# Performance work log

Hardware: AMD Instinct MI355X
Metric: run time of the kernel (lower is better)

## Reference

```python
import jax, jax.numpy as jnp
import numpy as np

N, E, F_IN, H, G, C = 50000, 600000, 128, 128, 500, 10


def _lin(k, fi, fo):
    # Glorot-ish scaled init for a [fi, fo] weight
    return (jax.random.normal(k, (fi, fo), jnp.float32) / np.float32(np.sqrt(fi)))


def setup_inputs() -> dict:
    key = jax.random.key(0)
    ks = jax.random.split(key, 16)
    x = jax.random.normal(ks[0], (N, F_IN), jnp.float32)
    edge_index = jax.random.randint(ks[1], (2, E), 0, N, dtype=jnp.int32)
    batch = jnp.sort(jax.random.randint(ks[2], (N,), 0, G, dtype=jnp.int32))
    return {
        "x": x, "edge_index": edge_index, "batch": batch,
        # SAGEConv i: out = mean_aggr @ Wl + bl + x @ Wr  (PyG default: mean aggr, root weight, bias on lin_l)
        "Wl1": _lin(ks[3], F_IN, H), "bl1": jnp.zeros((H,), jnp.float32), "Wr1": _lin(ks[4], F_IN, H),
        "Wl2": _lin(ks[5], H, H),    "bl2": jnp.zeros((H,), jnp.float32), "Wr2": _lin(ks[6], H, H),
        "Wl3": _lin(ks[7], H, H),    "bl3": jnp.zeros((H,), jnp.float32), "Wr3": _lin(ks[8], H, H),
        "W4": _lin(ks[9], H, 64), "b4": jnp.zeros((64,), jnp.float32),
        "W5": _lin(ks[10], 64, C), "b5": jnp.zeros((C,), jnp.float32),
    }


def _segment_mean(vals, ids, num_segments):
    s = jax.ops.segment_sum(vals, ids, num_segments=num_segments)
    cnt = jax.ops.segment_sum(jnp.ones((vals.shape[0], 1), vals.dtype), ids, num_segments=num_segments)
    return s / jnp.maximum(cnt, 1.0)


def _sage_conv(x, src, dst, Wl, bl, Wr):
    # gather source features along edges, mean-aggregate at destinations
    aggr = _segment_mean(x[src], dst, N)  # [N, F]
    return aggr @ Wl + bl + x @ Wr


def reference(x, edge_index, batch, Wl1, bl1, Wr1, Wl2, bl2, Wr2, Wl3, bl3, Wr3, W4, b4, W5, b5):
    src, dst = edge_index[0], edge_index[1]
    h = jax.nn.relu(_sage_conv(x, src, dst, Wl1, bl1, Wr1))
    h = jax.nn.relu(_sage_conv(h, src, dst, Wl2, bl2, Wr2))
    h = jax.nn.relu(_sage_conv(h, src, dst, Wl3, bl3, Wr3))
    g = _segment_mean(h, batch, G)          # global mean pool -> [G, H]
    g = jax.nn.relu(g @ W4 + b4)
    return jax.nn.log_softmax(g @ W5 + b5, axis=-1)
```

## Files before the change

kernel.cpp:

```cpp
#include <hip/hip_runtime.h>
#include <hip/hip_bf16.h>
#include <math.h>

#define FH 128

typedef __attribute__((ext_vector_type(8))) short short8v;
typedef __attribute__((ext_vector_type(4))) float float4v;
typedef unsigned short ushort_t;
typedef unsigned int   uint32;

__device__ __forceinline__ ushort_t f2bf(float f) {
    uint32 u = __builtin_bit_cast(uint32, f);
    u += 0x7fffu + ((u >> 16) & 1u);
    return (ushort_t)(u >> 16);
}
__device__ __forceinline__ float bf_lo(uint32 w) { return __builtin_bit_cast(float, w << 16); }
__device__ __forceinline__ float bf_hi(uint32 w) { return __builtin_bit_cast(float, w & 0xffff0000u); }
__device__ __forceinline__ uint32 pack2(float lo, float hi) {
    return (uint32)f2bf(lo) | ((uint32)f2bf(hi) << 16);
}

__device__ __forceinline__ void pack_one(const float* __restrict__ Wl,
                                         const float* __restrict__ Wr,
                                         ushort_t* __restrict__ Bp, int t) {
    int k = t >> 7, n = t & 127;
    float v = (k < FH) ? Wl[k * FH + n] : Wr[(k - FH) * FH + n];
    int nt = n >> 4, kt = k >> 5;
    int lane = (n & 15) + (((k >> 3) & 3) << 4);
    int j = k & 7;
    Bp[(((nt * 8 + kt) * 64) + lane) * 8 + j] = f2bf(v);
}

__global__ __launch_bounds__(256) void prep_kernel(const float* __restrict__ x,
                                                   ushort_t* __restrict__ xb, size_t n,
                                                   int cvtBlocks,
                                                   const float* __restrict__ Wl1, const float* __restrict__ Wr1, ushort_t* __restrict__ Bp1,
                                                   const float* __restrict__ Wl2, const float* __restrict__ Wr2, ushort_t* __restrict__ Bp2,
                                                   const float* __restrict__ Wl3, const float* __restrict__ Wr3, ushort_t* __restrict__ Bp3) {
    int b = blockIdx.x;
    if (b < cvtBlocks) {
        size_t base = ((size_t)b * 256 + threadIdx.x) * 8;
        if (base >= n) return;
        const float4 a = *(const float4*)(x + base);
        const float4 c = *(const float4*)(x + base + 4);
        ushort_t o[8] = {f2bf(a.x), f2bf(a.y), f2bf(a.z), f2bf(a.w),
                         f2bf(c.x), f2bf(c.y), f2bf(c.z), f2bf(c.w)};
        *(uint4*)(xb + base) = *(const uint4*)o;
    } else {
        int pb = b - cvtBlocks;
        int which = pb >> 7;
        int t = (pb & 127) * 256 + threadIdx.x;
        if (which == 0)      pack_one(Wl1, Wr1, Bp1, t);
        else if (which == 1) pack_one(Wl2, Wr2, Bp2, t);
        else                 pack_one(Wl3, Wr3, Bp3, t);
    }
}

__global__ __launch_bounds__(256) void deg_kernel(const int* __restrict__ dst,
                                                  int* __restrict__ deg, int E) {
    int e = blockIdx.x * 256 + threadIdx.x;
    if (e < E) atomicAdd(&deg[dst[e]], 1);
}

__global__ __launch_bounds__(256) void scan1_kernel(const int* __restrict__ deg,
                                                    int* __restrict__ rowptr,
                                                    int* __restrict__ blockSums, int N) {
    __shared__ int lds[256];
    const int base = blockIdx.x * 1024;
    const int t = threadIdx.x;
    int v[4]; int sum = 0;
    #pragma unroll
    for (int j = 0; j < 4; ++j) {
        int idx = base + t * 4 + j;
        v[j] = (idx < N) ? deg[idx] : 0;
        sum += v[j];
    }
    lds[t] = sum; __syncthreads();
    for (int off = 1; off < 256; off <<= 1) {
        int val = lds[t];
        int add = (t >= off) ? lds[t - off] : 0;
        __syncthreads();
        lds[t] = val + add;
        __syncthreads();
    }
    int run = (t > 0) ? lds[t - 1] : 0;
    #pragma unroll
    for (int j = 0; j < 4; ++j) {
        int idx = base + t * 4 + j;
        if (idx < N) rowptr[idx] = run;
        run += v[j];
    }
    if (t == 255) blockSums[blockIdx.x] = lds[255];
}

__global__ void scan2_kernel(int* __restrict__ blockSums, int* __restrict__ rowptr,
                             int nb, int N) {
    if (threadIdx.x == 0 && blockIdx.x == 0) {
        int carry = 0;
        for (int i = 0; i < nb; ++i) {
            int s = blockSums[i];
            blockSums[i] = carry;
            carry += s;
        }
        rowptr[N] = carry;
    }
}

__global__ __launch_bounds__(256) void scan3_kernel(int* __restrict__ rowptr,
                                                    int* __restrict__ pos,
                                                    const int* __restrict__ blockSums, int N) {
    const int base = blockIdx.x * 1024;
    const int add = blockSums[blockIdx.x];
    #pragma unroll
    for (int j = 0; j < 4; ++j) {
        int idx = base + threadIdx.x * 4 + j;
        if (idx < N) {
            int v = rowptr[idx] + add;
            rowptr[idx] = v;
            pos[idx] = v;
        }
    }
}

__global__ __launch_bounds__(256) void fill_csr_kernel(const int* __restrict__ src,
                                                       const int* __restrict__ dst,
                                                       int* __restrict__ pos,
                                                       int* __restrict__ csr, int E) {
    int e = blockIdx.x * 256 + threadIdx.x;
    if (e >= E) return;
    int idx = atomicAdd(&pos[dst[e]], 1);
    csr[idx] = src[e];
}

__global__ __launch_bounds__(256) void group_bounds_kernel(const int* __restrict__ batch,
                                                           int* __restrict__ gstart,
                                                           int N, int G) {
    int g = blockIdx.x * 256 + threadIdx.x;
    if (g > G) return;
    int lo = 0, hi = N;
    while (lo < hi) {
        int mid = (lo + hi) >> 1;
        if (batch[mid] < g) lo = mid + 1; else hi = mid;
    }
    gstart[g] = lo;
}

__global__ __launch_bounds__(256) void pull_mean_kernel(const ushort_t* __restrict__ x,
                                                        const int* __restrict__ rowptr,
                                                        const int* __restrict__ csr,
                                                        ushort_t* __restrict__ aggr, int N) {
    const int v = (blockIdx.x * 256 + threadIdx.x) >> 6;
    if (v >= N) return;
    const int lane = threadIdx.x & 63;
    const int grp  = lane >> 4;
    const int li   = lane & 15;
    const int beg = rowptr[v], end = rowptr[v + 1];
    const uint4* xp = (const uint4*)x + li;

    float a0 = 0.f, a1 = 0.f, a2 = 0.f, a3 = 0.f;
    float a4 = 0.f, a5 = 0.f, a6 = 0.f, a7 = 0.f;

    int i = beg + grp;
    for (; i + 4 < end; i += 8) {
        const int s0 = csr[i];
        const int s1 = csr[i + 4];
        const uint4 w0 = xp[(size_t)s0 * 16];
        const uint4 w1 = xp[(size_t)s1 * 16];
        a0 += bf_lo(w0.x); a1 += bf_hi(w0.x); a2 += bf_lo(w0.y); a3 += bf_hi(w0.y);
        a4 += bf_lo(w0.z); a5 += bf_hi(w0.z); a6 += bf_lo(w0.w); a7 += bf_hi(w0.w);
        a0 += bf_lo(w1.x); a1 += bf_hi(w1.x); a2 += bf_lo(w1.y); a3 += bf_hi(w1.y);
        a4 += bf_lo(w1.z); a5 += bf_hi(w1.z); a6 += bf_lo(w1.w); a7 += bf_hi(w1.w);
    }
    if (i < end) {
        const int s0 = csr[i];
        const uint4 w0 = xp[(size_t)s0 * 16];
        a0 += bf_lo(w0.x); a1 += bf_hi(w0.x); a2 += bf_lo(w0.y); a3 += bf_hi(w0.y);
        a4 += bf_lo(w0.z); a5 += bf_hi(w0.z); a6 += bf_lo(w0.w); a7 += bf_hi(w0.w);
    }

    a0 += __shfl_xor(a0, 16); a1 += __shfl_xor(a1, 16);
    a2 += __shfl_xor(a2, 16); a3 += __shfl_xor(a3, 16);
    a4 += __shfl_xor(a4, 16); a5 += __shfl_xor(a5, 16);
    a6 += __shfl_xor(a6, 16); a7 += __shfl_xor(a7, 16);
    a0 += __shfl_xor(a0, 32); a1 += __shfl_xor(a1, 32);
    a2 += __shfl_xor(a2, 32); a3 += __shfl_xor(a3, 32);
    a4 += __shfl_xor(a4, 32); a5 += __shfl_xor(a5, 32);
    a6 += __shfl_xor(a6, 32); a7 += __shfl_xor(a7, 32);

    if (grp == 0) {
        const float inv = 1.0f / (float)max(end - beg, 1);
        uint4 o;
        o.x = pack2(a0 * inv, a1 * inv);
        o.y = pack2(a2 * inv, a3 * inv);
        o.z = pack2(a4 * inv, a5 * inv);
        o.w = pack2(a6 * inv, a7 * inv);
        ((uint4*)aggr)[(size_t)v * 16 + li] = o;
    }
}

__global__ __launch_bounds__(256) void sage_mfma_kernel(const ushort_t* __restrict__ xin,
                                                        const ushort_t* __restrict__ aggr,
                                                        const ushort_t* __restrict__ Bp,
                                                        const float* __restrict__ bl,
                                                        ushort_t* __restrict__ out, int M) {
    __shared__ ushort_t sB[8 * 8 * 64 * 8];
    const int tid = threadIdx.x;
    {
        const uint4* s = (const uint4*)Bp;
        uint4* d = (uint4*)sB;
        #pragma unroll
        for (int i = 0; i < 16; ++i)
            d[tid + 256 * i] = s[tid + 256 * i];
    }
    __syncthreads();

    const int wave = tid >> 6;
    const int lane = tid & 63;
    const int grp  = lane >> 4;
    const int rowBase = (blockIdx.x * 4 + wave) * 16;
    if (rowBase >= M) return;
    const int arow = min(rowBase + (lane & 15), M - 1);

    short8v afrag[8];
    #pragma unroll
    for (int kt = 0; kt < 4; ++kt)
        afrag[kt] = *(const short8v*)(aggr + (size_t)arow * FH + kt * 32 + grp * 8);
    #pragma unroll
    for (int kt = 0; kt < 4; ++kt)
        afrag[4 + kt] = *(const short8v*)(xin + (size_t)arow * FH + kt * 32 + grp * 8);

    #pragma unroll
    for (int nt = 0; nt < 8; ++nt) {
        float4v acc = {0.f, 0.f, 0.f, 0.f};
        #pragma unroll
        for (int kt = 0; kt < 8; ++kt) {
            const short8v b = *(const short8v*)(sB + (((nt * 8 + kt) * 64) + lane) * 8);
            acc = __builtin_amdgcn_mfma_f32_16x16x32_bf16(afrag[kt], b, acc, 0, 0, 0);
        }
        const int col = nt * 16 + (lane & 15);
        const float bias = bl[col];
        #pragma unroll
        for (int r = 0; r < 4; ++r) {
            const int row = rowBase + grp * 4 + r;
            if (row < M)
                out[(size_t)row * FH + col] = f2bf(fmaxf(acc[r] + bias, 0.f));
        }
    }
}

__global__ __launch_bounds__(256) void head_kernel(const ushort_t* __restrict__ h,
                                                   const int* __restrict__ gstart,
                                                   const float* __restrict__ W4,
                                                   const float* __restrict__ b4,
                                                   const float* __restrict__ W5,
                                                   const float* __restrict__ b5,
                                                   float* __restrict__ out, int G) {
    __shared__ float sred[4][FH];
    __shared__ float sg2[64];
    __shared__ float sl[10];
    __shared__ float slse;
    const int g = blockIdx.x;
    const int t = threadIdx.x;
    const int wave = t >> 6, lane = t & 63;
    const int beg = gstart[g], end = gstart[g + 1];

    const uint32* hp = (const uint32*)h + lane;
    float a0 = 0.f, a1 = 0.f;
    for (int i = beg + wave; i < end; i += 4) {
        const uint32 w = hp[(size_t)i * 64];
        a0 += bf_lo(w); a1 += bf_hi(w);
    }
    sred[wave][lane * 2]     = a0;
    sred[wave][lane * 2 + 1] = a1;
    __syncthreads();
    if (t < FH) {
        const float s = sred[0][t] + sred[1][t] + sred[2][t] + sred[3][t];
        sred[0][t] = s / (float)max(end - beg, 1);
    }
    __syncthreads();
    if (t < 64) {
        float acc = b4[t];
        #pragma unroll 4
        for (int k = 0; k < FH; ++k)
            acc += sred[0][k] * W4[k * 64 + t];
        sg2[t] = fmaxf(acc, 0.f);
    }
    __syncthreads();
    if (t < 10) {
        float acc = b5[t];
        #pragma unroll 4
        for (int k = 0; k < 64; ++k)
            acc += sg2[k] * W5[k * 10 + t];
        sl[t] = acc;
    }
    __syncthreads();
    if (t == 0) {
        float m = sl[0];
        #pragma unroll
        for (int j = 1; j < 10; ++j) m = fmaxf(m, sl[j]);
        float s = 0.f;
        #pragma unroll
        for (int j = 0; j < 10; ++j) s += expf(sl[j] - m);
        slse = m + logf(s);
    }
    __syncthreads();
    if (t < 10) out[g * 10 + t] = sl[t] - slse;
}

extern "C" void kernel_launch(void* const* d_in, const int* in_sizes, int n_in,
                              void* d_out, int out_size, void* d_ws, size_t ws_size,
                              hipStream_t stream) {
    const float* x     = (const float*)d_in[0];
    const int*   ei    = (const int*)d_in[1];
    const int*   batch = (const int*)d_in[2];
    const float* Wl1 = (const float*)d_in[3];
    const float* bl1 = (const float*)d_in[4];
    const float* Wr1 = (const float*)d_in[5];
    const float* Wl2 = (const float*)d_in[6];
    const float* bl2 = (const float*)d_in[7];
    const float* Wr2 = (const float*)d_in[8];
    const float* Wl3 = (const float*)d_in[9];
    const float* bl3 = (const float*)d_in[10];
    const float* Wr3 = (const float*)d_in[11];
    const float* W4  = (const float*)d_in[12];
    const float* b4  = (const float*)d_in[13];
    const float* W5  = (const float*)d_in[14];
    const float* b5  = (const float*)d_in[15];
    float* out = (float*)d_out;

    const int N = in_sizes[0] / FH;
    const int E = in_sizes[1] / 2;
    const int G = out_size / 10;
    const int* src = ei;
    const int* dst = ei + E;

    char* p = (char*)d_ws;
    auto take = [&](size_t bytes) { char* q = p; p += (bytes + 255) & ~(size_t)255; return q; };
    ushort_t* xb    = (ushort_t*)take((size_t)N * FH * 2);
    ushort_t* h     = (ushort_t*)take((size_t)N * FH * 2);
    ushort_t* aggrb = (ushort_t*)take((size_t)N * FH * 2);
    int* deg        = (int*)take((size_t)N * 4);
    int* rowptr     = (int*)take((size_t)(N + 1) * 4);
    int* pos        = (int*)take((size_t)N * 4);
    int* csr        = (int*)take((size_t)E * 4);
    int* blockSums  = (int*)take(256 * 4);
    ushort_t* Bp1   = (ushort_t*)take(256 * FH * 2);
    ushort_t* Bp2   = (ushort_t*)take(256 * FH * 2);
    ushort_t* Bp3   = (ushort_t*)take(256 * FH * 2);
    int* gstart     = (int*)take((size_t)(G + 1) * 4);

    const int nb = (N + 1023) / 1024;

    hipMemsetAsync(deg, 0, (size_t)N * 4, stream);

    const int cvtBlocks = (int)(((size_t)N * FH / 8 + 255) / 256);
    prep_kernel<<<cvtBlocks + 384, 256, 0, stream>>>(x, xb, (size_t)N * FH, cvtBlocks,
                                                     Wl1, Wr1, Bp1, Wl2, Wr2, Bp2, Wl3, Wr3, Bp3);

    deg_kernel<<<(E + 255) / 256, 256, 0, stream>>>(dst, deg, E);
    scan1_kernel<<<nb, 256, 0, stream>>>(deg, rowptr, blockSums, N);
    scan2_kernel<<<1, 64, 0, stream>>>(blockSums, rowptr, nb, N);
    scan3_kernel<<<nb, 256, 0, stream>>>(rowptr, pos, blockSums, N);
    fill_csr_kernel<<<(E + 255) / 256, 256, 0, stream>>>(src, dst, pos, csr, E);

    group_bounds_kernel<<<(G + 256) / 256, 256, 0, stream>>>(batch, gstart, N, G);

    const int pullGrid = (N * 64 + 255) / 256;
    const int gemmGrid = (N + 63) / 64;

    pull_mean_kernel<<<pullGrid, 256, 0, stream>>>(xb, rowptr, csr, aggrb, N);
    sage_mfma_kernel<<<gemmGrid, 256, 0, stream>>>(xb, aggrb, Bp1, bl1, h, N);

    pull_mean_kernel<<<pullGrid, 256, 0, stream>>>(h, rowptr, csr, aggrb, N);
    sage_mfma_kernel<<<gemmGrid, 256, 0, stream>>>(h, aggrb, Bp2, bl2, h, N);

    pull_mean_kernel<<<pullGrid, 256, 0, stream>>>(h, rowptr, csr, aggrb, N);
    sage_mfma_kernel<<<gemmGrid, 256, 0, stream>>>(h, aggrb, Bp3, bl3, h, N);

    head_kernel<<<G, 256, 0, stream>>>(h, gstart, W4, b4, W5, b5, out, G);
}
```

Before: 242.9 us.

## Fuse setup kernels, prefetch gathers in pull-mean, stage GEMM output through LDS

Folds the degree-count and group-bounds kernels into the prep kernel to cut launches. The pull-mean aggregation now issues up to four independent neighbour gathers per lane group before accumulating, to raise memory-level parallelism for typical degrees. The MFMA kernel keeps all output tiles in registers, then writes bias+ReLU results into LDS and stores full 16-byte rows for coalesced global writes. This costs a block barrier and more accumulator registers.

New measurement: 219.6 us. 9.6% less time.

```diff
diff --git a/kernel.cpp b/kernel.cpp
--- a/kernel.cpp
+++ b/kernel.cpp
@@ -31,12 +31,13 @@
     Bp[(((nt * 8 + kt) * 64) + lane) * 8 + j] = f2bf(v);
 }
 
-__global__ __launch_bounds__(256) void prep_kernel(const float* __restrict__ x,
-                                                   ushort_t* __restrict__ xb, size_t n,
-                                                   int cvtBlocks,
-                                                   const float* __restrict__ Wl1, const float* __restrict__ Wr1, ushort_t* __restrict__ Bp1,
-                                                   const float* __restrict__ Wl2, const float* __restrict__ Wr2, ushort_t* __restrict__ Bp2,
-                                                   const float* __restrict__ Wl3, const float* __restrict__ Wr3, ushort_t* __restrict__ Bp3) {
+__global__ __launch_bounds__(256) void fused_prep_kernel(
+        const float* __restrict__ x, ushort_t* __restrict__ xb, size_t n, int cvtBlocks,
+        const float* __restrict__ Wl1, const float* __restrict__ Wr1, ushort_t* __restrict__ Bp1,
+        const float* __restrict__ Wl2, const float* __restrict__ Wr2, ushort_t* __restrict__ Bp2,
+        const float* __restrict__ Wl3, const float* __restrict__ Wr3, ushort_t* __restrict__ Bp3,
+        const int* __restrict__ dst, int* __restrict__ deg, int E, int degBlocks,
+        const int* __restrict__ batch, int* __restrict__ gstart, int N, int G) {
     int b = blockIdx.x;
     if (b < cvtBlocks) {
         size_t base = ((size_t)b * 256 + threadIdx.x) * 8;
@@ -46,20 +47,34 @@
         ushort_t o[8] = {f2bf(a.x), f2bf(a.y), f2bf(a.z), f2bf(a.w),
                          f2bf(c.x), f2bf(c.y), f2bf(c.z), f2bf(c.w)};
         *(uint4*)(xb + base) = *(const uint4*)o;
-    } else {
-        int pb = b - cvtBlocks;
-        int which = pb >> 7;
-        int t = (pb & 127) * 256 + threadIdx.x;
+        return;
+    }
+    b -= cvtBlocks;
+    if (b < 384) {
+        int which = b >> 7;
+        int t = (b & 127) * 256 + threadIdx.x;
         if (which == 0)      pack_one(Wl1, Wr1, Bp1, t);
         else if (which == 1) pack_one(Wl2, Wr2, Bp2, t);
         else                 pack_one(Wl3, Wr3, Bp3, t);
-    }
-}
-
-__global__ __launch_bounds__(256) void deg_kernel(const int* __restrict__ dst,
-                                                  int* __restrict__ deg, int E) {
-    int e = blockIdx.x * 256 + threadIdx.x;
-    if (e < E) atomicAdd(&deg[dst[e]], 1);
+        return;
+    }
+    b -= 384;
+    if (b < degBlocks) {
+        int e = b * 256 + threadIdx.x;
+        if (e < E) atomicAdd(&deg[dst[e]], 1);
+        return;
+    }
+    b -= degBlocks;
+    {
+        int g = b * 256 + threadIdx.x;
+        if (g > G) return;
+        int lo = 0, hi = N;
+        while (lo < hi) {
+            int mid = (lo + hi) >> 1;
+            if (batch[mid] < g) lo = mid + 1; else hi = mid;
+        }
+        gstart[g] = lo;
+    }
 }
 
 __global__ __launch_bounds__(256) void scan1_kernel(const int* __restrict__ deg,
@@ -130,19 +145,6 @@
     if (e >= E) return;
     int idx = atomicAdd(&pos[dst[e]], 1);
     csr[idx] = src[e];
-}
-
-__global__ __launch_bounds__(256) void group_bounds_kernel(const int* __restrict__ batch,
-                                                           int* __restrict__ gstart,
-                                                           int N, int G) {
-    int g = blockIdx.x * 256 + threadIdx.x;
-    if (g > G) return;
-    int lo = 0, hi = N;
-    while (lo < hi) {
-        int mid = (lo + hi) >> 1;
-        if (batch[mid] < g) lo = mid + 1; else hi = mid;
-    }
-    gstart[g] = lo;
 }
 
 __global__ __launch_bounds__(256) void pull_mean_kernel(const ushort_t* __restrict__ x,
@@ -157,25 +159,27 @@
     const int beg = rowptr[v], end = rowptr[v + 1];
     const uint4* xp = (const uint4*)x + li;
 
-    float a0 = 0.f, a1 = 0.f, a2 = 0.f, a3 = 0.f;
-    float a4 = 0.f, a5 = 0.f, a6 = 0.f, a7 = 0.f;
-
-    int i = beg + grp;
-    for (; i + 4 < end; i += 8) {
-        const int s0 = csr[i];
-        const int s1 = csr[i + 4];
-        const uint4 w0 = xp[(size_t)s0 * 16];
-        const uint4 w1 = xp[(size_t)s1 * 16];
-        a0 += bf_lo(w0.x); a1 += bf_hi(w0.x); a2 += bf_lo(w0.y); a3 += bf_hi(w0.y);
-        a4 += bf_lo(w0.z); a5 += bf_hi(w0.z); a6 += bf_lo(w0.w); a7 += bf_hi(w0.w);
-        a0 += bf_lo(w1.x); a1 += bf_hi(w1.x); a2 += bf_lo(w1.y); a3 += bf_hi(w1.y);
-        a4 += bf_lo(w1.z); a5 += bf_hi(w1.z); a6 += bf_lo(w1.w); a7 += bf_hi(w1.w);
-    }
-    if (i < end) {
-        const int s0 = csr[i];
-        const uint4 w0 = xp[(size_t)s0 * 16];
-        a0 += bf_lo(w0.x); a1 += bf_hi(w0.x); a2 += bf_lo(w0.y); a3 += bf_hi(w0.y);
-        a4 += bf_lo(w0.z); a5 += bf_hi(w0.z); a6 += bf_lo(w0.w); a7 += bf_hi(w0.w);
+    const uint4 z = {0u, 0u, 0u, 0u};
+    uint4 w0 = z, w1 = z, w2 = z, w3 = z;
+    const int i0 = beg + grp;
+    if (i0 < end)      w0 = xp[(size_t)csr[i0] * 16];
+    if (i0 + 4 < end)  w1 = xp[(size_t)csr[i0 + 4] * 16];
+    if (i0 + 8 < end)  w2 = xp[(size_t)csr[i0 + 8] * 16];
+    if (i0 + 12 < end) w3 = xp[(size_t)csr[i0 + 12] * 16];
+
+    float a0 = (bf_lo(w0.x) + bf_lo(w1.x)) + (bf_lo(w2.x) + bf_lo(w3.x));
+    float a1 = (bf_hi(w0.x) + bf_hi(w1.x)) + (bf_hi(w2.x) + bf_hi(w3.x));
+    float a2 = (bf_lo(w0.y) + bf_lo(w1.y)) + (bf_lo(w2.y) + bf_lo(w3.y));
+    float a3 = (bf_hi(w0.y) + bf_hi(w1.y)) + (bf_hi(w2.y) + bf_hi(w3.y));
+    float a4 = (bf_lo(w0.z) + bf_lo(w1.z)) + (bf_lo(w2.z) + bf_lo(w3.z));
+    float a5 = (bf_hi(w0.z) + bf_hi(w1.z)) + (bf_hi(w2.z) + bf_hi(w3.z));
+    float a6 = (bf_lo(w0.w) + bf_lo(w1.w)) + (bf_lo(w2.w) + bf_lo(w3.w));
+    float a7 = (bf_hi(w0.w) + bf_hi(w1.w)) + (bf_hi(w2.w) + bf_hi(w3.w));
+
+    for (int i = beg + 16 + grp; i < end; i += 4) {
+        const uint4 w = xp[(size_t)csr[i] * 16];
+        a0 += bf_lo(w.x); a1 += bf_hi(w.x); a2 += bf_lo(w.y); a3 += bf_hi(w.y);
+        a4 += bf_lo(w.z); a5 += bf_hi(w.z); a6 += bf_lo(w.w); a7 += bf_hi(w.w);
     }
 
     a0 += __shfl_xor(a0, 16); a1 += __shfl_xor(a1, 16);
@@ -198,12 +202,13 @@
     }
 }
 
+#define SO_STRIDE 136
 __global__ __launch_bounds__(256) void sage_mfma_kernel(const ushort_t* __restrict__ xin,
                                                         const ushort_t* __restrict__ aggr,
                                                         const ushort_t* __restrict__ Bp,
                                                         const float* __restrict__ bl,
                                                         ushort_t* __restrict__ out, int M) {
-    __shared__ ushort_t sB[8 * 8 * 64 * 8];
+    __shared__ ushort_t sB[32768];
     const int tid = threadIdx.x;
     {
         const uint4* s = (const uint4*)Bp;
@@ -217,9 +222,9 @@
     const int wave = tid >> 6;
     const int lane = tid & 63;
     const int grp  = lane >> 4;
+    const int li   = lane & 15;
     const int rowBase = (blockIdx.x * 4 + wave) * 16;
-    if (rowBase >= M) return;
-    const int arow = min(rowBase + (lane & 15), M - 1);
+    const int arow = min(rowBase + li, M - 1);
 
     short8v afrag[8];
     #pragma unroll
@@ -229,21 +234,36 @@
     for (int kt = 0; kt < 4; ++kt)
         afrag[4 + kt] = *(const short8v*)(xin + (size_t)arow * FH + kt * 32 + grp * 8);
 
+    float4v acc[8];
     #pragma unroll
     for (int nt = 0; nt < 8; ++nt) {
-        float4v acc = {0.f, 0.f, 0.f, 0.f};
+        acc[nt] = (float4v){0.f, 0.f, 0.f, 0.f};
         #pragma unroll
         for (int kt = 0; kt < 8; ++kt) {
             const short8v b = *(const short8v*)(sB + (((nt * 8 + kt) * 64) + lane) * 8);
-            acc = __builtin_amdgcn_mfma_f32_16x16x32_bf16(afrag[kt], b, acc, 0, 0, 0);
+            acc[nt] = __builtin_amdgcn_mfma_f32_16x16x32_bf16(afrag[kt], b, acc[nt], 0, 0, 0);
         }
-        const int col = nt * 16 + (lane & 15);
-        const float bias = bl[col];
+    }
+
+    __syncthreads();
+
+    ushort_t* so = sB + wave * (16 * SO_STRIDE);
+    #pragma unroll
+    for (int nt = 0; nt < 8; ++nt) {
+        const float bias = bl[nt * 16 + li];
         #pragma unroll
-        for (int r = 0; r < 4; ++r) {
-            const int row = rowBase + grp * 4 + r;
-            if (row < M)
-                out[(size_t)row * FH + col] = f2bf(fmaxf(acc[r] + bias, 0.f));
+        for (int r = 0; r < 4; ++r)
+            so[(grp * 4 + r) * SO_STRIDE + nt * 16 + li] = f2bf(fmaxf(acc[nt][r] + bias, 0.f));
+    }
+    #pragma unroll
+    for (int t = 0; t < 4; ++t) {
+        const int idx = lane + 64 * t;
+        const int r  = idx >> 4;
+        const int ch = idx & 15;
+        const int row = rowBase + r;
+        if (row < M) {
+            const uint4 val = *(const uint4*)(so + r * SO_STRIDE + ch * 8);
+            *(uint4*)(out + (size_t)row * FH + ch * 8) = val;
         }
     }
 }
@@ -354,17 +374,19 @@
     hipMemsetAsync(deg, 0, (size_t)N * 4, stream);
 
     const int cvtBlocks = (int)(((size_t)N * FH / 8 + 255) / 256);
-    prep_kernel<<<cvtBlocks + 384, 256, 0, stream>>>(x, xb, (size_t)N * FH, cvtBlocks,
-                                                     Wl1, Wr1, Bp1, Wl2, Wr2, Bp2, Wl3, Wr3, Bp3);
-
-    deg_kernel<<<(E + 255) / 256, 256, 0, stream>>>(dst, deg, E);
+    const int degBlocks = (E + 255) / 256;
+    const int gbBlocks  = (G + 1 + 255) / 256;
+    fused_prep_kernel<<<cvtBlocks + 384 + degBlocks + gbBlocks, 256, 0, stream>>>(
+        x, xb, (size_t)N * FH, cvtBlocks,
+        Wl1, Wr1, Bp1, Wl2, Wr2, Bp2, Wl3, Wr3, Bp3,
+        dst, deg, E, degBlocks,
+        batch, gstart, N, G);
+
     scan1_kernel<<<nb, 256, 0, stream>>>(deg, rowptr, blockSums, N);
     scan2_kernel<<<1, 64, 0, stream>>>(blockSums, rowptr, nb, N);
     scan3_kernel<<<nb, 256, 0, stream>>>(rowptr, pos, blockSums, N);
     fill_csr_kernel<<<(E + 255) / 256, 256, 0, stream>>>(src, dst, pos, csr, E);
 
-    group_bounds_kernel<<<(G + 256) / 256, 256, 0, stream>>>(batch, gstart, N, G);
-
     const int pullGrid = (N * 64 + 255) / 256;
     const int gemmGrid = (N + 63) / 64;
 
```
